# Kernel tuning notes

Measured on AMD Instinct MI355X. Metric: run time of the kernel, lower is better.

The kernel has to match this reference:

```python
import jax, jax.numpy as jnp
import numpy as np

N, C, T, V = 64, 256, 64, 25
K, VN, RR = 8, 5, 4            # num_subset, virtual_num, rel_reduction
VT = V + VN                    # 30 vertices incl. virtual joints
Cg = C // K                    # 32 in-channels per group
H = max(1, Cg // RR)           # 8 hidden channels for to_v / to_w
O = 256                        # out_channels
Og = O // K                    # 32 out-channels per group
TOPK = min(9, VT)


def setup_inputs() -> dict:
    key = jax.random.key(0)
    ks = jax.random.split(key, 8)
    f = jnp.float32
    rn = lambda k, s, sc=1.0: jax.random.normal(k, s, dtype=f) * sc
    return {
        "x": rn(ks[0], (N, C, T, V)),
        "adjacency": jax.random.uniform(ks[1], (K, VT, VT), dtype=f),   # fixed graph buffer
        "edge_importance": jnp.ones((K, VT, VT), f),
        "hyper_joint": rn(ks[2], (VN, C)),
        "alpha": jnp.ones((1,), f),
        "to_v_w": rn(ks[3], (K, H, Cg), 0.05), "to_v_b": jnp.zeros((K, H), f),
        "to_w1_w": rn(ks[4], (K, H, Cg), 0.05), "to_w1_b": jnp.zeros((K, H), f),
        "to_w2_w": rn(ks[5], (K, K * H), 0.05), "to_w2_b": jnp.zeros((K,), f),
        "conv_d_w": rn(ks[6], (K, Og, Cg), 0.05), "conv_d_b": jnp.zeros((K, Og), f),
        "bn_gamma": jnp.full((O,), 1e-6, f), "bn_beta": jnp.zeros((O,), f),
    }


def _forward(x, adjacency, edge_importance, hyper_joint, alpha,
             to_v_w, to_v_b, to_w1_w, to_w1_b, to_w2_w, to_w2_b,
             conv_d_w, conv_d_b, bn_gamma, bn_beta):
    n, c, t, v = x.shape
    vn = hyper_joint.shape[0]
    vt = v + vn
    # append virtual joints along vertex dim: (n,c,t,v+vn)
    hx = jnp.broadcast_to(hyper_joint.T[None, :, None, :], (n, c, t, vn))
    xv = jnp.concatenate([x, hx], axis=-1)
    # a_norm: L1 row-normalize the weighted static adjacency (K,vt,vt)
    adj = edge_importance * adjacency
    adj = adj / (jnp.sum(jnp.abs(adj), axis=2, keepdims=True) + 1e-8)
    # --- hyper branch ---
    pooled = xv.mean(axis=2)                 # (n,c,vt) temporal mean pool
    pg = pooled.reshape(n, K, Cg, vt)        # grouped channels
    # to_v: grouped 1x1 conv1d, then permute -> (n,K,vt,H)
    vproj = jnp.einsum('nkcv,khc->nkvh', pg, to_v_w) + to_v_b[None, :, None, :]
    # cdist with zero-safe sqrt (grad 0 at coincident points, like torch.cdist)
    diff = vproj[:, :, :, None, :] - vproj[:, :, None, :, :]   # (n,K,vt,vt,H)
    d2 = jnp.sum(diff * diff, axis=-1)
    nz = d2 > 0
    dist = jnp.sqrt(jnp.where(nz, d2, 1.0)) * nz
    # topk smallest distances, softmax over negated values, scatter to incidence
    neg_vals, idx = jax.lax.top_k(-dist, TOPK)
    probs = jax.nn.softmax(neg_vals, axis=-1)                  # softmax(-topk_dist)
    incidence = jnp.sum(jax.nn.one_hot(idx, vt, dtype=x.dtype) * probs[..., None], axis=3)  # (n,K,vt,vt)
    # to_w: grouped conv -> leaky_relu -> full conv -> tanh, -> (n,K,vt)
    w1 = jax.nn.leaky_relu(jnp.einsum('nkcv,khc->nkhv', pg, to_w1_w) + to_w1_b[None, :, :, None])
    weights = jnp.tanh(jnp.einsum('nqv,kq->nkv', w1.reshape(n, K * H, vt), to_w2_w) + to_w2_b[None, :, None])
    # hyper_norm: inc_w @ diag(w/norm_w) @ inc^T expressed as elementwise scaling
    d = weights / (jnp.sum(jnp.abs(incidence), axis=2) + 1e-8)             # diag(w)/norm_w diagonal
    inc_w = incidence * weights[:, :, None, :]
    inc_w = inc_w / (jnp.sum(jnp.abs(inc_w), axis=3, keepdims=True) + 1e-8)
    hyper_adj = jnp.einsum('nkuv,nkv,nkwv->nkuw', inc_w, d, incidence)
    adj_full = adj[None] + jax.nn.relu(alpha)[0] * hyper_adj               # (n,K,vt,vt)
    # conv_d: grouped 1x1 conv2d -> (n,K,Og,t,vt)
    xg = xv.reshape(n, K, Cg, t, vt)
    dense = jnp.einsum('nkctv,koc->nkotv', xg, conv_d_w) + conv_d_b[None, :, :, None, None]
    # adjacency-weighted graph conv
    y = jnp.einsum('nkuv,nkotv->nkotu', adj_full, dense).reshape(n, O, t, vt)
    y = y[..., :v]
    residual = x  # in_channels == out_channels -> down is None; xv[...,:v] == x
    # BatchNorm2d (eval: running mean 0, var 1, eps 1e-5; gamma init 1e-6)
    scale = bn_gamma / jnp.sqrt(1.0 + 1e-5)
    y = y * scale[None, :, None, None] + bn_beta[None, :, None, None]
    return jax.nn.relu(y + residual)


def reference(x, adjacency, edge_importance, hyper_joint, alpha,
              to_v_w, to_v_b, to_w1_w, to_w1_b, to_w2_w, to_w2_b,
              conv_d_w, conv_d_b, bn_gamma, bn_beta):
    y = _forward(x, adjacency, edge_importance, hyper_joint, alpha,
                 to_v_w, to_v_b, to_w1_w, to_w1_b, to_w2_w, to_w2_b,
                 conv_d_w, conv_d_b, bn_gamma, bn_beta)
    return (y, hyper_joint)
```

## Files before the change

### kernel.cpp

```cpp
#include <hip/hip_runtime.h>
#include <hip/hip_bf16.h>

#define N_ 64
#define C_ 256
#define T_ 64
#define V_ 25
#define K_ 8
#define VN_ 5
#define VT_ 30
#define CG_ 32
#define H_ 8
#define O_ 256
#define OG_ 32
#define TOPK_ 9

typedef __attribute__((ext_vector_type(8))) short short8;
typedef __attribute__((ext_vector_type(4))) float f32x4;

__device__ __forceinline__ short bfbits(float f) {
    union { __hip_bfloat16 h; short s; } cv;
    cv.h = __float2bfloat16(f);
    return cv.s;
}
__device__ __forceinline__ short8 mk8(f32x4 a, f32x4 b) {
    short8 r;
    r[0] = bfbits(a[0]); r[1] = bfbits(a[1]); r[2] = bfbits(a[2]); r[3] = bfbits(a[3]);
    r[4] = bfbits(b[0]); r[5] = bfbits(b[1]); r[6] = bfbits(b[2]); r[7] = bfbits(b[3]);
    return r;
}
__device__ __forceinline__ short8 mk8f(const float* v) {
    short8 r;
    #pragma unroll
    for (int j = 0; j < 8; ++j) r[j] = bfbits(v[j]);
    return r;
}
__device__ __forceinline__ unsigned pkbf(float a, float b) {
    return (unsigned)(unsigned short)bfbits(a) | ((unsigned)(unsigned short)bfbits(b) << 16);
}

__global__ __launch_bounds__(256) void k_pool(const float* __restrict__ x,
                                              const float* __restrict__ hyper,
                                              float* __restrict__ pooled,
                                              float* __restrict__ out_tail) {
    __shared__ float ls[6400];
    int b = blockIdx.x;
    int tid = threadIdx.x;
    if (b >= N_ * 64) {
        for (int i = tid; i < VN_ * C_; i += 256) out_tail[i] = hyper[i];
        return;
    }
    int n = b >> 6, c0 = (b & 63) * 4;
    const float4* xp = (const float4*)(x + (size_t)(n * C_ + c0) * (T_ * V_));
    for (int i = tid; i < 1600; i += 256) ((float4*)ls)[i] = xp[i];
    __syncthreads();
    if (tid < 100) {
        int c_l = tid / 25, v = tid % 25;
        const float* p = ls + c_l * 1600 + v;
        float s = 0.f;
        #pragma unroll
        for (int t = 0; t < T_; ++t) s += p[t * 25];
        pooled[(size_t)(n * C_ + c0 + c_l) * 25 + v] = s * (1.0f / T_);
    }
}

__global__ __launch_bounds__(256) void k_graph(
    const float* __restrict__ pooled, const float* __restrict__ hyper,
    const float* __restrict__ adjc, const float* __restrict__ edge,
    const float* __restrict__ alpha,
    const float* __restrict__ to_v_w, const float* __restrict__ to_v_b,
    const float* __restrict__ to_w1_w, const float* __restrict__ to_w1_b,
    const float* __restrict__ to_w2_w, const float* __restrict__ to_w2_b,
    float* __restrict__ adjR) {
    __shared__ float smem[12000];
    float* vproj = smem;
    float* w1s   = smem + 1920;
    float* pg    = smem + 3840;
    float* inc   = smem + 3840;
    float* wt    = smem + 11040;
    float* gv    = smem + 11280;
    float* rs    = smem + 11520;
    float* rsA   = smem + 11760;

    int n = blockIdx.x;
    int tid = threadIdx.x;
    for (int i = tid; i < C_ * V_; i += 256) {
        int c = i / V_, v = i % V_;
        pg[c * VT_ + v] = pooled[(size_t)n * C_ * V_ + i];
    }
    for (int i = tid; i < C_ * VN_; i += 256) {
        int c = i / VN_, j = i % VN_;
        pg[c * VT_ + V_ + j] = hyper[j * C_ + c];
    }
    __syncthreads();

    for (int i = tid; i < K_ * VT_ * H_; i += 256) {
        int k = i / (VT_ * H_);
        int r = i % (VT_ * H_);
        int v = r / H_, h = r % H_;
        const float* w = to_v_w + (k * H_ + h) * CG_;
        const float* pgk = pg + (k * CG_) * VT_ + v;
        float s = 0.f;
        #pragma unroll
        for (int c = 0; c < CG_; ++c) s += pgk[c * VT_] * w[c];
        vproj[(k * VT_ + v) * H_ + h] = s + to_v_b[k * H_ + h];
    }
    for (int i = tid; i < K_ * H_ * VT_; i += 256) {
        int k = i / (H_ * VT_);
        int r = i % (H_ * VT_);
        int h = r / VT_, v = r % VT_;
        const float* w = to_w1_w + (k * H_ + h) * CG_;
        const float* pgk = pg + (k * CG_) * VT_ + v;
        float s = 0.f;
        #pragma unroll
        for (int c = 0; c < CG_; ++c) s += pgk[c * VT_] * w[c];
        s += to_w1_b[k * H_ + h];
        w1s[(k * H_ + h) * VT_ + v] = (s > 0.f) ? s : 0.01f * s;
    }
    __syncthreads();

    if (tid < K_ * VT_) {
        int k = tid / VT_;
        float s = to_w2_b[k];
        #pragma unroll
        for (int q = 0; q < K_ * H_; ++q)
            s += w1s[q * VT_ + (tid % VT_)] * to_w2_w[k * K_ * H_ + q];
        wt[tid] = tanhf(s);
        float sa = 0.f;
        const float* ea = edge + (size_t)tid * VT_;
        const float* aa = adjc + (size_t)tid * VT_;
        #pragma unroll
        for (int w2 = 0; w2 < VT_; ++w2) sa += fabsf(ea[w2] * aa[w2]);
        rsA[tid] = sa + 1e-8f;
    }
    if (tid < K_ * VT_) {
        int k = tid / VT_, u = tid % VT_;
        const float* vu = vproj + (k * VT_ + u) * H_;
        float nd[VT_];
        #pragma unroll
        for (int v = 0; v < VT_; ++v) {
            const float* vv = vproj + (k * VT_ + v) * H_;
            float d2 = 0.f;
            #pragma unroll
            for (int h = 0; h < H_; ++h) { float df = vu[h] - vv[h]; d2 += df * df; }
            nd[v] = (d2 > 0.f) ? -sqrtf(d2) : 0.0f;
        }
        unsigned taken = 0;
        float vals[TOPK_]; int ids[TOPK_];
        for (int j = 0; j < TOPK_; ++j) {
            float best = -3.4e38f; int bi = 0;
            #pragma unroll
            for (int v = 0; v < VT_; ++v) {
                if (!((taken >> v) & 1u) && nd[v] > best) { best = nd[v]; bi = v; }
            }
            vals[j] = best; ids[j] = bi; taken |= (1u << bi);
        }
        float m = vals[0], se = 0.f, e[TOPK_];
        #pragma unroll
        for (int j = 0; j < TOPK_; ++j) { e[j] = expf(vals[j] - m); se += e[j]; }
        float invse = 1.f / se;
        float* row = inc + (size_t)tid * VT_;
        #pragma unroll
        for (int v = 0; v < VT_; ++v) row[v] = 0.f;
        for (int j = 0; j < TOPK_; ++j) row[ids[j]] = e[j] * invse;
    }
    __syncthreads();

    if (tid < K_ * VT_) {
        int k = tid / VT_, v = tid % VT_;
        float cs = 0.f;
        #pragma unroll
        for (int u = 0; u < VT_; ++u) cs += fabsf(inc[(k * VT_ + u) * VT_ + v]);
        float d = wt[tid] / (cs + 1e-8f);
        gv[tid] = wt[tid] * d;
        float s = 0.f;
        const float* row = inc + (size_t)tid * VT_;
        const float* w = wt + k * VT_;
        #pragma unroll
        for (int vv = 0; vv < VT_; ++vv) s += fabsf(row[vv] * w[vv]);
        rs[tid] = s + 1e-8f;
    }
    __syncthreads();

    float ar = alpha[0]; ar = ar > 0.f ? ar : 0.f;
    int kk = tid >> 5, uu = tid & 31;
    size_t obase = (size_t)n * K_ * 1024 + (size_t)kk * 1024 + (size_t)uu * 32;
    if (uu < VT_) {
        const float* ru = inc + (kk * VT_ + uu) * VT_;
        const float* g  = gv + kk * VT_;
        float tu[VT_];
        #pragma unroll
        for (int vv = 0; vv < VT_; ++vv) tu[vv] = ru[vv] * g[vv];
        float inv_rs = 1.0f / rs[kk * VT_ + uu];
        float inv_rsA = 1.0f / rsA[kk * VT_ + uu];
        for (int v = 0; v < 32; ++v) {
            float val = 0.f;
            if (v < VT_) {
                const float* rw = inc + (kk * VT_ + v) * VT_;
                float s = 0.f;
                #pragma unroll
                for (int vv = 0; vv < VT_; ++vv) s += tu[vv] * rw[vv];
                int ei = (kk * VT_ + uu) * VT_ + v;
                val = edge[ei] * adjc[ei] * inv_rsA + ar * (s * inv_rs);
            }
            adjR[obase + v] = val;
        }
    } else {
        #pragma unroll
        for (int v = 0; v < 32; ++v) adjR[obase + v] = 0.f;
    }
}

__global__ __launch_bounds__(256, 4) void k_main(
    const float* __restrict__ x, const float* __restrict__ hyper,
    const float* __restrict__ adjR,
    const float* __restrict__ conv_w, const float* __restrict__ conv_b,
    const float* __restrict__ gamma, const float* __restrict__ beta,
    float* __restrict__ out) {
    __shared__ __align__(16) float xs[32 * 132];
    __shared__ __align__(16) unsigned Mb[4 * 32 * 18];

    int b = blockIdx.x;
    int tc = b & 15, k = (b >> 4) & 7, n = b >> 7;
    int tid = threadIdx.x;
    int w = tid >> 6;
    int lane = tid & 63;
    int qd = lane >> 4;
    int l16 = lane & 15;

    const float* xg = x + ((size_t)(n * C_ + k * CG_) * T_ + tc * 4) * V_;
    #pragma unroll
    for (int ii = 0; ii < 4; ++ii) {
        int i = tid + ii * 256;
        if (i < 800) {
            int c = i / 25, col = i % 25;
            f32x4 f4 = *(const f32x4*)(xg + (size_t)c * (T_ * V_) + col * 4);
            *(f32x4*)(xs + c * 132 + col * 4) = f4;
        }
    }

    short8 Wf[2];
    #pragma unroll
    for (int mi = 0; mi < 2; ++mi) {
        const float* wp = conv_w + (size_t)(k * OG_ + 16 * mi + l16) * CG_ + qd * 8;
        Wf[mi] = mk8(*(const f32x4*)wp, *(const f32x4*)(wp + 4));
    }
    short8 Bf[2]; float Su[2];
    #pragma unroll
    for (int ni = 0; ni < 2; ++ni) {
        const float* ap = adjR + (((size_t)(n * K_ + k)) * 32 + 16 * ni + l16) * 32 + qd * 8;
        f32x4 a0 = *(const f32x4*)ap, a1 = *(const f32x4*)(ap + 4);
        Bf[ni] = mk8(a0, a1);
        float s = a0[0] + a0[1] + a0[2] + a0[3] + a1[0] + a1[1] + a1[2] + a1[3];
        s += __shfl_xor(s, 16);
        s += __shfl_xor(s, 32);
        Su[ni] = s;
    }
    f32x4 cb4[2], sc4[2], bt4[2];
    #pragma unroll
    for (int mi = 0; mi < 2; ++mi) {
        int o0 = k * OG_ + 16 * mi + qd * 4;
        cb4[mi] = *(const f32x4*)(conv_b + o0);
        f32x4 g = *(const f32x4*)(gamma + o0);
        #pragma unroll
        for (int r = 0; r < 4; ++r) g[r] *= 0.999995000037f;
        sc4[mi] = g;
        bt4[mi] = *(const f32x4*)(beta + o0);
    }
    short8 Ht[2];
    #pragma unroll
    for (int mi = 0; mi < 2; ++mi) {
        int c = k * CG_ + 16 * mi + l16;
        short8 h;
        h[0] = 0; h[6] = 0; h[7] = 0;
        #pragma unroll
        for (int j = 0; j < 5; ++j) h[1 + j] = bfbits(hyper[j * C_ + c]);
        Ht[mi] = h;
    }

    __syncthreads();

    unsigned* Mbw = Mb + w * (32 * 18);

    short8 Ax[2];
    #pragma unroll
    for (int mi = 0; mi < 2; ++mi) {
        const float* xp = xs + (16 * mi + l16) * 132 + w * 25;
        if (qd < 3) {
            float va[8];
            #pragma unroll
            for (int j = 0; j < 8; ++j) va[j] = xp[qd * 8 + j];
            Ax[mi] = mk8f(va);
        } else {
            short8 h = Ht[mi];
            h[0] = bfbits(xp[24]);
            Ax[mi] = h;
        }
    }
    f32x4 CM[2][2];
    #pragma unroll
    for (int mi = 0; mi < 2; ++mi)
        #pragma unroll
        for (int ni = 0; ni < 2; ++ni) {
            f32x4 z = {0.f, 0.f, 0.f, 0.f};
            CM[mi][ni] = __builtin_amdgcn_mfma_f32_16x16x32_bf16(Ax[mi], Bf[ni], z, 0, 0, 0);
        }
    #pragma unroll
    for (int mi = 0; mi < 2; ++mi)
        #pragma unroll
        for (int ni = 0; ni < 2; ++ni) {
            int u = 16 * ni + l16;
            uint2 pr;
            pr.x = pkbf(CM[mi][ni][0], CM[mi][ni][1]);
            pr.y = pkbf(CM[mi][ni][2], CM[mi][ni][3]);
            *(uint2*)(Mbw + u * 18 + 8 * mi + 2 * qd) = pr;
        }
    short8 Bm[2];
    #pragma unroll
    for (int ni = 0; ni < 2; ++ni) {
        int u = 16 * ni + l16;
        uint2 lo = *(const uint2*)(Mbw + u * 18 + qd * 4);
        uint2 hi = *(const uint2*)(Mbw + u * 18 + qd * 4 + 2);
        union { unsigned uu[4]; short8 s; } bm;
        bm.uu[0] = lo.x; bm.uu[1] = lo.y; bm.uu[2] = hi.x; bm.uu[3] = hi.y;
        Bm[ni] = bm.s;
    }
    f32x4 CY[2][2];
    #pragma unroll
    for (int mi = 0; mi < 2; ++mi)
        #pragma unroll
        for (int ni = 0; ni < 2; ++ni) {
            f32x4 z = {0.f, 0.f, 0.f, 0.f};
            CY[mi][ni] = __builtin_amdgcn_mfma_f32_16x16x32_bf16(Wf[mi], Bm[ni], z, 0, 0, 0);
        }
    #pragma unroll
    for (int ni = 0; ni < 2; ++ni) {
        int u = 16 * ni + l16;
        if (u < V_) {
            #pragma unroll
            for (int mi = 0; mi < 2; ++mi) {
                #pragma unroll
                for (int r = 0; r < 4; ++r) {
                    float* rp = xs + (16 * mi + qd * 4 + r) * 132 + w * 25 + u;
                    float res = *rp;
                    float val = (CY[mi][ni][r] + cb4[mi][r] * Su[ni]) * sc4[mi][r]
                                + bt4[mi][r] + res;
                    *rp = val > 0.f ? val : 0.f;
                }
            }
        }
    }

    __syncthreads();

    float* og = out + ((size_t)(n * C_ + k * CG_) * T_ + tc * 4) * V_;
    #pragma unroll
    for (int ii = 0; ii < 4; ++ii) {
        int i = tid + ii * 256;
        if (i < 800) {
            int c = i / 25, col = i % 25;
            f32x4 f4 = *(const f32x4*)(xs + c * 132 + col * 4);
            __builtin_nontemporal_store(f4, (f32x4*)(og + (size_t)c * (T_ * V_) + col * 4));
        }
    }
}

extern "C" void kernel_launch(void* const* d_in, const int* in_sizes, int n_in,
                              void* d_out, int out_size, void* d_ws, size_t ws_size,
                              hipStream_t stream) {
    const float* x     = (const float*)d_in[0];
    const float* adjc  = (const float*)d_in[1];
    const float* edge  = (const float*)d_in[2];
    const float* hyper = (const float*)d_in[3];
    const float* alpha = (const float*)d_in[4];
    const float* tvw   = (const float*)d_in[5];
    const float* tvb   = (const float*)d_in[6];
    const float* t1w   = (const float*)d_in[7];
    const float* t1b   = (const float*)d_in[8];
    const float* t2w   = (const float*)d_in[9];
    const float* t2b   = (const float*)d_in[10];
    const float* cw    = (const float*)d_in[11];
    const float* cb    = (const float*)d_in[12];
    const float* gam   = (const float*)d_in[13];
    const float* bet   = (const float*)d_in[14];
    float* out = (float*)d_out;

    float* pooled = (float*)d_ws;
    float* adjR   = pooled + N_ * C_ * V_;

    k_pool<<<dim3(N_ * 64 + 1), dim3(256), 0, stream>>>(
        x, hyper, pooled, out + (size_t)N_ * O_ * T_ * V_);
    k_graph<<<dim3(N_), dim3(256), 0, stream>>>(
        pooled, hyper, adjc, edge, alpha, tvw, tvb, t1w, t1b, t2w, t2b, adjR);
    k_main<<<dim3(N_ * K_ * 16), dim3(256), 0, stream>>>(
        x, hyper, adjR, cw, cb, gam, bet, out);
}
```

Measured before the change: 288.9 us.

## Split graph kernel across (batch, subset) blocks for more parallelism

The adjacency-building kernel now launches one block per (sample, subset) pair instead of one per sample, so each block handles only one of the K subsets. Per-block work shrinks and the small serial phases (top-k, tanh weights, row sums) run in separate thread ranges at the same time, and the final adjacency output is computed fully in parallel over all 1024 entries. The cost is that each block reloads the whole pooled tile and recomputes the to_w1 projection for all subsets, since the tanh weights need every subset's hidden features.

```diff
diff --git a/kernel.cpp b/kernel.cpp
--- a/kernel.cpp
+++ b/kernel.cpp
@@ -71,18 +71,16 @@
     const float* __restrict__ to_w1_w, const float* __restrict__ to_w1_b,
     const float* __restrict__ to_w2_w, const float* __restrict__ to_w2_b,
     float* __restrict__ adjR) {
-    __shared__ float smem[12000];
-    float* vproj = smem;
-    float* w1s   = smem + 1920;
-    float* pg    = smem + 3840;
-    float* inc   = smem + 3840;
-    float* wt    = smem + 11040;
-    float* gv    = smem + 11280;
-    float* rs    = smem + 11520;
-    float* rsA   = smem + 11760;
-
-    int n = blockIdx.x;
+    __shared__ float pg[C_ * VT_];
+    __shared__ float w1s[K_ * H_ * VT_];
+    __shared__ float vproj[VT_ * H_];
+    __shared__ float inc[VT_ * VT_];
+    __shared__ float wt30[VT_], gv30[VT_], rs30[VT_], rsA30[VT_];
+
+    int b = blockIdx.x;
+    int n = b >> 3, k = b & 7;
     int tid = threadIdx.x;
+
     for (int i = tid; i < C_ * V_; i += 256) {
         int c = i / V_, v = i % V_;
         pg[c * VT_ + v] = pooled[(size_t)n * C_ * V_ + i];
@@ -93,52 +91,35 @@
     }
     __syncthreads();
 
-    for (int i = tid; i < K_ * VT_ * H_; i += 256) {
-        int k = i / (VT_ * H_);
-        int r = i % (VT_ * H_);
-        int v = r / H_, h = r % H_;
+    if (tid < VT_ * H_) {
+        int v = tid / H_, h = tid % H_;
         const float* w = to_v_w + (k * H_ + h) * CG_;
         const float* pgk = pg + (k * CG_) * VT_ + v;
         float s = 0.f;
         #pragma unroll
         for (int c = 0; c < CG_; ++c) s += pgk[c * VT_] * w[c];
-        vproj[(k * VT_ + v) * H_ + h] = s + to_v_b[k * H_ + h];
+        vproj[v * H_ + h] = s + to_v_b[k * H_ + h];
     }
     for (int i = tid; i < K_ * H_ * VT_; i += 256) {
-        int k = i / (H_ * VT_);
-        int r = i % (H_ * VT_);
-        int h = r / VT_, v = r % VT_;
-        const float* w = to_w1_w + (k * H_ + h) * CG_;
-        const float* pgk = pg + (k * CG_) * VT_ + v;
+        int q = i / VT_, v = i % VT_;
+        int k2 = q / H_;
+        const float* w = to_w1_w + q * CG_;
+        const float* pgk = pg + (k2 * CG_) * VT_ + v;
         float s = 0.f;
         #pragma unroll
         for (int c = 0; c < CG_; ++c) s += pgk[c * VT_] * w[c];
-        s += to_w1_b[k * H_ + h];
-        w1s[(k * H_ + h) * VT_ + v] = (s > 0.f) ? s : 0.01f * s;
-    }
-    __syncthreads();
-
-    if (tid < K_ * VT_) {
-        int k = tid / VT_;
-        float s = to_w2_b[k];
-        #pragma unroll
-        for (int q = 0; q < K_ * H_; ++q)
-            s += w1s[q * VT_ + (tid % VT_)] * to_w2_w[k * K_ * H_ + q];
-        wt[tid] = tanhf(s);
-        float sa = 0.f;
-        const float* ea = edge + (size_t)tid * VT_;
-        const float* aa = adjc + (size_t)tid * VT_;
-        #pragma unroll
-        for (int w2 = 0; w2 < VT_; ++w2) sa += fabsf(ea[w2] * aa[w2]);
-        rsA[tid] = sa + 1e-8f;
-    }
-    if (tid < K_ * VT_) {
-        int k = tid / VT_, u = tid % VT_;
-        const float* vu = vproj + (k * VT_ + u) * H_;
+        s += to_w1_b[q];
+        w1s[q * VT_ + v] = (s > 0.f) ? s : 0.01f * s;
+    }
+    __syncthreads();
+
+    if (tid < VT_) {
+        int u = tid;
+        const float* vu = vproj + u * H_;
         float nd[VT_];
         #pragma unroll
         for (int v = 0; v < VT_; ++v) {
-            const float* vv = vproj + (k * VT_ + v) * H_;
+            const float* vv = vproj + v * H_;
             float d2 = 0.f;
             #pragma unroll
             for (int h = 0; h < H_; ++h) { float df = vu[h] - vv[h]; d2 += df * df; }
@@ -158,55 +139,64 @@
         #pragma unroll
         for (int j = 0; j < TOPK_; ++j) { e[j] = expf(vals[j] - m); se += e[j]; }
         float invse = 1.f / se;
-        float* row = inc + (size_t)tid * VT_;
+        float* row = inc + u * VT_;
         #pragma unroll
         for (int v = 0; v < VT_; ++v) row[v] = 0.f;
         for (int j = 0; j < TOPK_; ++j) row[ids[j]] = e[j] * invse;
-    }
-    __syncthreads();
-
-    if (tid < K_ * VT_) {
-        int k = tid / VT_, v = tid % VT_;
+    } else if (tid >= 64 && tid < 64 + VT_) {
+        int v = tid - 64;
+        float s = to_w2_b[k];
+        #pragma unroll
+        for (int q = 0; q < K_ * H_; ++q)
+            s += w1s[q * VT_ + v] * to_w2_w[k * K_ * H_ + q];
+        wt30[v] = tanhf(s);
+    } else if (tid >= 128 && tid < 128 + VT_) {
+        int u = tid - 128;
+        float sa = 0.f;
+        const float* ea = edge + (size_t)(k * VT_ + u) * VT_;
+        const float* aa = adjc + (size_t)(k * VT_ + u) * VT_;
+        #pragma unroll
+        for (int w2 = 0; w2 < VT_; ++w2) sa += fabsf(ea[w2] * aa[w2]);
+        rsA30[u] = sa + 1e-8f;
+    }
+    __syncthreads();
+
+    if (tid < VT_) {
+        int v = tid;
         float cs = 0.f;
         #pragma unroll
-        for (int u = 0; u < VT_; ++u) cs += fabsf(inc[(k * VT_ + u) * VT_ + v]);
-        float d = wt[tid] / (cs + 1e-8f);
-        gv[tid] = wt[tid] * d;
+        for (int u = 0; u < VT_; ++u) cs += fabsf(inc[u * VT_ + v]);
+        float d = wt30[v] / (cs + 1e-8f);
+        gv30[v] = wt30[v] * d;
+    } else if (tid >= 64 && tid < 64 + VT_) {
+        int u = tid - 64;
         float s = 0.f;
-        const float* row = inc + (size_t)tid * VT_;
-        const float* w = wt + k * VT_;
-        #pragma unroll
-        for (int vv = 0; vv < VT_; ++vv) s += fabsf(row[vv] * w[vv]);
-        rs[tid] = s + 1e-8f;
+        const float* row = inc + u * VT_;
+        #pragma unroll
+        for (int vv = 0; vv < VT_; ++vv) s += fabsf(row[vv] * wt30[vv]);
+        rs30[u] = s + 1e-8f;
     }
     __syncthreads();
 
     float ar = alpha[0]; ar = ar > 0.f ? ar : 0.f;
-    int kk = tid >> 5, uu = tid & 31;
-    size_t obase = (size_t)n * K_ * 1024 + (size_t)kk * 1024 + (size_t)uu * 32;
-    if (uu < VT_) {
-        const float* ru = inc + (kk * VT_ + uu) * VT_;
-        const float* g  = gv + kk * VT_;
-        float tu[VT_];
-        #pragma unroll
-        for (int vv = 0; vv < VT_; ++vv) tu[vv] = ru[vv] * g[vv];
-        float inv_rs = 1.0f / rs[kk * VT_ + uu];
-        float inv_rsA = 1.0f / rsA[kk * VT_ + uu];
-        for (int v = 0; v < 32; ++v) {
-            float val = 0.f;
-            if (v < VT_) {
-                const float* rw = inc + (kk * VT_ + v) * VT_;
-                float s = 0.f;
-                #pragma unroll
-                for (int vv = 0; vv < VT_; ++vv) s += tu[vv] * rw[vv];
-                int ei = (kk * VT_ + uu) * VT_ + v;
-                val = edge[ei] * adjc[ei] * inv_rsA + ar * (s * inv_rs);
-            }
-            adjR[obase + v] = val;
-        }
-    } else {
-        #pragma unroll
-        for (int v = 0; v < 32; ++v) adjR[obase + v] = 0.f;
+    size_t obase = (size_t)b * 1024;
+    #pragma unroll
+    for (int ii = 0; ii < 4; ++ii) {
+        int i = tid + ii * 256;
+        int u = i >> 5, v = i & 31;
+        float val = 0.f;
+        if (u < VT_ && v < VT_) {
+            const float* ru = inc + u * VT_;
+            const float* rw = inc + v * VT_;
+            float s = 0.f;
+            #pragma unroll
+            for (int vv = 0; vv < VT_; ++vv) s += ru[vv] * gv30[vv] * rw[vv];
+            float inv_rs = 1.0f / rs30[u];
+            float inv_rsA = 1.0f / rsA30[u];
+            int ei = (k * VT_ + u) * VT_ + v;
+            val = edge[ei] * adjc[ei] * inv_rsA + ar * (s * inv_rs);
+        }
+        adjR[obase + i] = val;
     }
 }
 
@@ -389,7 +379,7 @@
 
     k_pool<<<dim3(N_ * 64 + 1), dim3(256), 0, stream>>>(
         x, hyper, pooled, out + (size_t)N_ * O_ * T_ * V_);
-    k_graph<<<dim3(N_), dim3(256), 0, stream>>>(
+    k_graph<<<dim3(N_ * K_), dim3(256), 0, stream>>>(
         pooled, hyper, adjc, edge, alpha, tvw, tvb, t1w, t1b, t2w, t2b, adjR);
     k_main<<<dim3(N_ * K_ * 16), dim3(256), 0, stream>>>(
         x, hyper, adjR, cw, cb, gam, bet, out);
```

Measured after the change: 269.0 us. -6.9%, faster.
